# Kernel optimization log

Hardware: AMD Instinct MI355X
Metric: run time of the kernel (lower is better)

The kernel has to match this reference:

```python
import jax, jax.numpy as jnp
import numpy as np
import math

N = 20000      # nodes
E = 640000     # edges (avg degree 32)
G = 128        # g_dim (input features)
H1 = 128       # rgcn output dim
H2 = 128       # transformer output dim
R = 8          # num_relations


def setup_inputs() -> dict:
    key = jax.random.key(0)
    ks = jax.random.split(key, 12)
    x = jax.random.normal(ks[0], (N, G), dtype=jnp.float32)
    edge_index = jax.random.randint(ks[1], (2, E), 0, N)
    edge_type = jax.random.randint(ks[2], (E,), 0, R)
    s_in = 1.0 / math.sqrt(G)
    s_h1 = 1.0 / math.sqrt(H1)
    return {
        'x': x,
        'edge_index': edge_index,
        'edge_type': edge_type,
        # RGCNConv params (per-relation weights + root weight + bias)
        'rgcn_weight': jax.random.normal(ks[3], (R, G, H1), dtype=jnp.float32) * s_in,
        'rgcn_root': jax.random.normal(ks[4], (G, H1), dtype=jnp.float32) * s_in,
        'rgcn_bias': jnp.zeros((H1,), dtype=jnp.float32),
        # TransformerConv params (heads=1): query/key/value + skip linear
        'Wq': jax.random.normal(ks[5], (H1, H2), dtype=jnp.float32) * s_h1,
        'bq': jnp.zeros((H2,), dtype=jnp.float32),
        'Wk': jax.random.normal(ks[6], (H1, H2), dtype=jnp.float32) * s_h1,
        'bk': jnp.zeros((H2,), dtype=jnp.float32),
        'Wv': jax.random.normal(ks[7], (H1, H2), dtype=jnp.float32) * s_h1,
        'bv': jnp.zeros((H2,), dtype=jnp.float32),
        'Ws': jax.random.normal(ks[8], (H1, H2), dtype=jnp.float32) * s_h1,
        'bs': jnp.zeros((H2,), dtype=jnp.float32),
    }


def reference(x, edge_index, edge_type, rgcn_weight, rgcn_root, rgcn_bias,
              Wq, bq, Wk, bk, Wv, bv, Ws, bs):
    n = x.shape[0]
    src, dst = edge_index[0], edge_index[1]

    # ---- RGCNConv (aggr='mean' per relation, root weight + bias) ----
    # transform nodes by every relation, then gather per-edge message
    xr = jnp.einsum('ni,rio->nro', x, rgcn_weight)          # [N, R, H1]
    msg = xr[src, edge_type]                                # [E, H1]
    # per (dst, relation) edge counts for mean aggregation
    cnt = jnp.zeros((n, rgcn_weight.shape[0]), x.dtype).at[dst, edge_type].add(1.0)
    denom = jnp.maximum(cnt[dst, edge_type], 1.0)[:, None]  # [E, 1]
    agg = jnp.zeros((n, rgcn_weight.shape[2]), x.dtype).at[dst].add(msg / denom)
    h = agg + x @ rgcn_root + rgcn_bias
    h = jax.nn.relu(h)

    # ---- TransformerConv (heads=1, concat, root_weight=True) ----
    d = Wq.shape[1]
    q = h @ Wq + bq                                          # [N, H2]
    k = h @ Wk + bk
    v = h @ Wv + bv
    score = jnp.sum(q[dst] * k[src], axis=-1) / math.sqrt(d) # [E]
    # softmax over incoming edges of each destination node
    smax = jax.ops.segment_max(score, dst, num_segments=n)   # [N]
    e = jnp.exp(score - smax[dst])                           # [E]
    den = jax.ops.segment_sum(e, dst, num_segments=n)        # [N]
    alpha = e / jnp.maximum(den[dst], 1e-16)                 # [E]
    out = jax.ops.segment_sum(alpha[:, None] * v[src], dst, num_segments=n)
    out = out + h @ Ws + bs                                  # skip connection
    return jax.nn.relu(out)
```

## Files before the change

### kernel.cpp

```cpp
#include <hip/hip_runtime.h>

typedef unsigned short u16;
typedef unsigned int u32;
typedef __attribute__((ext_vector_type(8))) short short8;
typedef __attribute__((ext_vector_type(4))) float f32x4;

#define NN 20000
#define EE 640000
#define SCAN_BLOCKS 80

__device__ inline u16 f2bf(float f) {
    u32 x = __float_as_uint(f);
    return (u16)((x + 0x7FFFu + ((x >> 16) & 1u)) >> 16);
}
__device__ inline float lo16(u32 w) { return __uint_as_float(w << 16); }
__device__ inline float hi16(u32 w) { return __uint_as_float(w & 0xFFFF0000u); }
__device__ inline u32 packbf(float a, float b) { return ((u32)f2bf(b) << 16) | (u32)f2bf(a); }

#define CT_N (EE / 8)
#define CX_N (NN * 32)
#define WP_N (128 * 1152 + 4 * 128 * 128 + 512)
__global__ __launch_bounds__(256) void prep_count(const int* __restrict__ ei,
                                                  const int* __restrict__ et,
                                                  int* __restrict__ cnt, int* __restrict__ rank,
                                                  const float* __restrict__ x,
                                                  const float* rw, const float* root,
                                                  const float* Wq, const float* Wk,
                                                  const float* Wv, const float* Ws,
                                                  const float* bq, const float* bk,
                                                  const float* bv, const float* bs,
                                                  u16* __restrict__ xb,
                                                  u16* wt1, u16* wt2, float* bcat) {
    int idx = blockIdx.x * 256 + threadIdx.x;
    if (idx < CT_N) {
#pragma unroll
        for (int j = 0; j < 8; j++) {
            int e = idx + j * CT_N;
            int dst = ei[EE + e];
            int r = et[e];
            rank[e] = atomicAdd(&cnt[dst * 8 + r], 1);
        }
        return;
    }
    idx -= CT_N;
    if (idx < CX_N) {
        float4 v = *(const float4*)(x + (size_t)idx * 4);
        uint2 o;
        o.x = packbf(v.x, v.y);
        o.y = packbf(v.z, v.w);
        *(uint2*)(xb + (size_t)idx * 4) = o;
        return;
    }
    idx -= CX_N;
    const int S1 = 128 * 1152, S2 = 4 * 128 * 128;
    if (idx < S1) {
        int o = idx / 1152, k = idx - o * 1152;
        float v = (k < 1024) ? rw[k * 128 + o] : root[(k - 1024) * 128 + o];
        wt1[idx] = f2bf(v);
    } else if (idx < S1 + S2) {
        int j = idx - S1;
        int y = j >> 14, rem = j & 16383, o = rem >> 7, i = rem & 127;
        const float* W = (y == 0) ? Wq : (y == 1) ? Wk : (y == 2) ? Wv : Ws;
        wt2[j] = f2bf(W[i * 128 + o]);
    } else if (idx < S1 + S2 + 512) {
        int j = idx - (S1 + S2);
        int y = j >> 7, c = j & 127;
        const float* b = (y == 0) ? bq : (y == 1) ? bk : (y == 2) ? bv : bs;
        bcat[j] = b[c];
    }
}

__global__ __launch_bounds__(256) void scan_phase1(const int* __restrict__ cnt,
                                                   int* __restrict__ deg_pref,
                                                   int* __restrict__ blk_sums) {
    __shared__ int lds[256];
    int t = threadIdx.x;
    int n = blockIdx.x * 256 + t;
    int d = 0;
    if (n < NN) {
        int4 c0 = *(const int4*)(cnt + n * 8);
        int4 c1 = *(const int4*)(cnt + n * 8 + 4);
        d = c0.x + c0.y + c0.z + c0.w + c1.x + c1.y + c1.z + c1.w;
    }
    lds[t] = d;
    __syncthreads();
    for (int o = 1; o < 256; o <<= 1) {
        int v = (t >= o) ? lds[t - o] : 0;
        __syncthreads();
        lds[t] += v;
        __syncthreads();
    }
    if (n < NN) deg_pref[n] = lds[t];
    if (t == 255) blk_sums[blockIdx.x] = lds[255];
}

__global__ __launch_bounds__(256) void scan_phase3(const int* __restrict__ cnt,
                                                   const int* __restrict__ deg_pref,
                                                   const int* __restrict__ blk_sums,
                                                   int* __restrict__ row_off,
                                                   int* __restrict__ srt) {
    __shared__ int bs_lds[128];
    int t = threadIdx.x;
    if (t < 128) {
        int v = (t < SCAN_BLOCKS) ? blk_sums[t] : 0;
        bs_lds[t] = v;
    }
    __syncthreads();
    if (t < 128) {
        for (int o = 1; o < 128; o <<= 1) {
            int a = (t >= o) ? bs_lds[t - o] : 0;
            __syncthreads();
            bs_lds[t] += a;
            __syncthreads();
        }
    } else {
        for (int o = 1; o < 128; o <<= 1) {
            __syncthreads();
            __syncthreads();
        }
    }
    int blk_excl = (blockIdx.x > 0) ? bs_lds[blockIdx.x - 1] : 0;
    int n = blockIdx.x * 256 + t;
    if (n >= NN) return;
    int4 c0 = *(const int4*)(cnt + n * 8);
    int4 c1 = *(const int4*)(cnt + n * 8 + 4);
    int deg = c0.x + c0.y + c0.z + c0.w + c1.x + c1.y + c1.z + c1.w;
    int start = blk_excl + deg_pref[n] - deg;
    row_off[n] = start;
    int sub = start;
    int o[8];
    o[0] = sub; sub += c0.x;
    o[1] = sub; sub += c0.y;
    o[2] = sub; sub += c0.z;
    o[3] = sub; sub += c0.w;
    o[4] = sub; sub += c1.x;
    o[5] = sub; sub += c1.y;
    o[6] = sub; sub += c1.z;
    o[7] = sub; sub += c1.w;
    *(int4*)(srt + n * 8) = make_int4(o[0], o[1], o[2], o[3]);
    *(int4*)(srt + n * 8 + 4) = make_int4(o[4], o[5], o[6], o[7]);
    if (n == NN - 1) row_off[NN] = sub;
}

__global__ void scatter_kernel(const int* __restrict__ ei, const int* __restrict__ et,
                               const int* __restrict__ srt, const int* __restrict__ rank,
                               int* __restrict__ es) {
    int base = blockIdx.x * 2048 + threadIdx.x;
#pragma unroll
    for (int j = 0; j < 8; j++) {
        int e = base + j * 256;
        if (e < EE) {
            int dst = ei[EE + e];
            int src = ei[e];
            int r = et[e];
            es[srt[dst * 8 + r] + rank[e]] = src;
        }
    }
}

__global__ __launch_bounds__(256) void gemm_rgcn_fused(const u16* __restrict__ xb,
                                                       const int* __restrict__ srt,
                                                       const int* __restrict__ cnt,
                                                       const int* __restrict__ es,
                                                       const u16* __restrict__ Bt1,
                                                       const float* __restrict__ bias1,
                                                       const u16* __restrict__ Wt2,
                                                       const float* __restrict__ bcat,
                                                       u16* __restrict__ Cq, u16* __restrict__ Ckv,
                                                       u16* __restrict__ Cs) {
    __shared__ u16 As[2][16 * 136];
    int tid = threadIdx.x;
    int w = tid >> 6;
    int lane = tid & 63;
    int quad = lane >> 4;
    int ml = lane & 15;
    int nq = w;
    int block_m = blockIdx.x * 16;

    int node_l = tid >> 4;
    int th = tid & 15;
    int db = th * 8;
    int gnode = block_m + node_l;

    const u16* bp0 = Bt1 + (long)(nq * 32 + ml) * 1152 + quad * 8;

    f32x4 acc[2];
#pragma unroll
    for (int i = 0; i < 2; i++) acc[i] = (f32x4){0.f, 0.f, 0.f, 0.f};

#pragma unroll 1
    for (int slot = 0; slot < 9; slot++) {
        short8 bf[4][2];
#pragma unroll
        for (int ks = 0; ks < 4; ks++)
#pragma unroll
            for (int nt = 0; nt < 2; nt++)
                bf[ks][nt] = *(const short8*)(bp0 + (long)nt * 16 * 1152 + slot * 128 + ks * 32);

        u16* dst = &As[slot & 1][node_l * 136 + db];
        if (slot < 8) {
            int c = cnt[gnode * 8 + slot];
            int p0 = srt[gnode * 8 + slot];
            float a0 = 0.f, a1 = 0.f, a2 = 0.f, a3 = 0.f, a4 = 0.f, a5 = 0.f, a6 = 0.f, a7 = 0.f;
            int i = 0;
            for (; i + 2 <= c; i += 2) {
                int s0 = es[p0 + i], s1 = es[p0 + i + 1];
                uint4 wa = *(const uint4*)(xb + (long)s0 * 128 + db);
                uint4 wb = *(const uint4*)(xb + (long)s1 * 128 + db);
                a0 += lo16(wa.x) + lo16(wb.x);
                a1 += hi16(wa.x) + hi16(wb.x);
                a2 += lo16(wa.y) + lo16(wb.y);
                a3 += hi16(wa.y) + hi16(wb.y);
                a4 += lo16(wa.z) + lo16(wb.z);
                a5 += hi16(wa.z) + hi16(wb.z);
                a6 += lo16(wa.w) + lo16(wb.w);
                a7 += hi16(wa.w) + hi16(wb.w);
            }
            if (i < c) {
                int s0 = es[p0 + i];
                uint4 wa = *(const uint4*)(xb + (long)s0 * 128 + db);
                a0 += lo16(wa.x); a1 += hi16(wa.x); a2 += lo16(wa.y); a3 += hi16(wa.y);
                a4 += lo16(wa.z); a5 += hi16(wa.z); a6 += lo16(wa.w); a7 += hi16(wa.w);
            }
            float inv = 1.0f / (float)(c > 1 ? c : 1);
            uint4 o0 = make_uint4(packbf(a0 * inv, a1 * inv), packbf(a2 * inv, a3 * inv),
                                  packbf(a4 * inv, a5 * inv), packbf(a6 * inv, a7 * inv));
            *(uint4*)dst = o0;
        } else {
            short8 val = *(const short8*)(xb + (long)gnode * 128 + db);
            *(short8*)dst = val;
        }
        __syncthreads();
        const u16* ab = &As[slot & 1][0];
#pragma unroll
        for (int ks = 0; ks < 4; ks++) {
            short8 af = *(const short8*)(ab + ml * 136 + ks * 32 + quad * 8);
            acc[0] = __builtin_amdgcn_mfma_f32_16x16x32_bf16(af, bf[ks][0], acc[0], 0, 0, 0);
            acc[1] = __builtin_amdgcn_mfma_f32_16x16x32_bf16(af, bf[ks][1], acc[1], 0, 0, 0);
        }
    }
    __syncthreads();

#pragma unroll
    for (int nt = 0; nt < 2; nt++) {
        int col = nq * 32 + nt * 16 + ml;
        float bv = bias1[col];
#pragma unroll
        for (int i = 0; i < 4; i++) {
            int r = quad * 4 + i;
            As[0][r * 136 + col] = f2bf(fmaxf(acc[nt][i] + bv, 0.f));
        }
    }
    __syncthreads();

#pragma unroll 1
    for (int y = 0; y < 4; y++) {
        const u16* wp = Wt2 + (long)y * 16384 + (long)(nq * 32 + ml) * 128 + quad * 8;
        short8 bf2[4][2];
#pragma unroll
        for (int ks = 0; ks < 4; ks++)
#pragma unroll
            for (int nt = 0; nt < 2; nt++)
                bf2[ks][nt] = *(const short8*)(wp + (long)nt * 16 * 128 + ks * 32);
        f32x4 acc2[2];
#pragma unroll
        for (int i = 0; i < 2; i++) acc2[i] = (f32x4){0.f, 0.f, 0.f, 0.f};
#pragma unroll
        for (int ks = 0; ks < 4; ks++) {
            short8 af = *(const short8*)(&As[0][ml * 136 + ks * 32 + quad * 8]);
            acc2[0] = __builtin_amdgcn_mfma_f32_16x16x32_bf16(af, bf2[ks][0], acc2[0], 0, 0, 0);
            acc2[1] = __builtin_amdgcn_mfma_f32_16x16x32_bf16(af, bf2[ks][1], acc2[1], 0, 0, 0);
        }
        u16* C;
        int ldc;
        if (y == 0) { C = Cq; ldc = 128; }
        else if (y == 1) { C = Ckv; ldc = 256; }
        else if (y == 2) { C = Ckv + 128; ldc = 256; }
        else { C = Cs; ldc = 128; }
#pragma unroll
        for (int nt = 0; nt < 2; nt++) {
            int col = nq * 32 + nt * 16 + ml;
            float bv = bcat[y * 128 + col];
#pragma unroll
            for (int i = 0; i < 4; i++) {
                int gr = block_m + quad * 4 + i;
                C[(long)gr * ldc + col] = f2bf(acc2[nt][i] + bv);
            }
        }
    }
}

__global__ __launch_bounds__(128) void attn_kernel(const u16* __restrict__ q,
                                                   const u16* __restrict__ kv,
                                                   const u16* __restrict__ skip,
                                                   const int* __restrict__ row_off,
                                                   const int* __restrict__ es,
                                                   float* __restrict__ out) {
    int node = blockIdx.x * 8 + (threadIdx.x >> 4);
    int lane = threadIdx.x & 15;
    if (node >= NN) return;
    int p0 = row_off[node], p1 = row_off[node + 1];
    uint4 qw = *(const uint4*)(q + (long)node * 128 + lane * 8);
    float q0 = lo16(qw.x), q1 = hi16(qw.x), q2 = lo16(qw.y), q3 = hi16(qw.y);
    float q4 = lo16(qw.z), q5 = hi16(qw.z), q6 = lo16(qw.w), q7 = hi16(qw.w);
    const float SC = 0.08838834764831845f;
    float l = 0.f;
    float a0 = 0.f, a1 = 0.f, a2 = 0.f, a3 = 0.f, a4 = 0.f, a5 = 0.f, a6 = 0.f, a7 = 0.f;
    int p = p0;
    for (; p + 4 <= p1; p += 4) {
        const u16* b0 = kv + (long)es[p] * 256 + lane * 8;
        const u16* b1 = kv + (long)es[p + 1] * 256 + lane * 8;
        const u16* b2 = kv + (long)es[p + 2] * 256 + lane * 8;
        const u16* b3 = kv + (long)es[p + 3] * 256 + lane * 8;
        uint4 k0 = *(const uint4*)b0;
        uint4 k1 = *(const uint4*)b1;
        uint4 k2 = *(const uint4*)b2;
        uint4 k3 = *(const uint4*)b3;
        uint4 v0 = *(const uint4*)(b0 + 128);
        uint4 v1 = *(const uint4*)(b1 + 128);
        uint4 v2 = *(const uint4*)(b2 + 128);
        uint4 v3 = *(const uint4*)(b3 + 128);
        float t0 = q0 * lo16(k0.x) + q1 * hi16(k0.x) + q2 * lo16(k0.y) + q3 * hi16(k0.y) +
                   q4 * lo16(k0.z) + q5 * hi16(k0.z) + q6 * lo16(k0.w) + q7 * hi16(k0.w);
        float t1 = q0 * lo16(k1.x) + q1 * hi16(k1.x) + q2 * lo16(k1.y) + q3 * hi16(k1.y) +
                   q4 * lo16(k1.z) + q5 * hi16(k1.z) + q6 * lo16(k1.w) + q7 * hi16(k1.w);
        float t2 = q0 * lo16(k2.x) + q1 * hi16(k2.x) + q2 * lo16(k2.y) + q3 * hi16(k2.y) +
                   q4 * lo16(k2.z) + q5 * hi16(k2.z) + q6 * lo16(k2.w) + q7 * hi16(k2.w);
        float t3 = q0 * lo16(k3.x) + q1 * hi16(k3.x) + q2 * lo16(k3.y) + q3 * hi16(k3.y) +
                   q4 * lo16(k3.z) + q5 * hi16(k3.z) + q6 * lo16(k3.w) + q7 * hi16(k3.w);
#pragma unroll
        for (int off = 8; off >= 1; off >>= 1) {
            t0 += __shfl_xor(t0, off, 16);
            t1 += __shfl_xor(t1, off, 16);
            t2 += __shfl_xor(t2, off, 16);
            t3 += __shfl_xor(t3, off, 16);
        }
        float w0 = __expf(fminf(t0 * SC, 70.f));
        float w1 = __expf(fminf(t1 * SC, 70.f));
        float w2 = __expf(fminf(t2 * SC, 70.f));
        float w3 = __expf(fminf(t3 * SC, 70.f));
        l += (w0 + w1) + (w2 + w3);
        a0 += w0 * lo16(v0.x) + w1 * lo16(v1.x) + w2 * lo16(v2.x) + w3 * lo16(v3.x);
        a1 += w0 * hi16(v0.x) + w1 * hi16(v1.x) + w2 * hi16(v2.x) + w3 * hi16(v3.x);
        a2 += w0 * lo16(v0.y) + w1 * lo16(v1.y) + w2 * lo16(v2.y) + w3 * lo16(v3.y);
        a3 += w0 * hi16(v0.y) + w1 * hi16(v1.y) + w2 * hi16(v2.y) + w3 * hi16(v3.y);
        a4 += w0 * lo16(v0.z) + w1 * lo16(v1.z) + w2 * lo16(v2.z) + w3 * lo16(v3.z);
        a5 += w0 * hi16(v0.z) + w1 * hi16(v1.z) + w2 * hi16(v2.z) + w3 * hi16(v3.z);
        a6 += w0 * lo16(v0.w) + w1 * lo16(v1.w) + w2 * lo16(v2.w) + w3 * lo16(v3.w);
        a7 += w0 * hi16(v0.w) + w1 * hi16(v1.w) + w2 * hi16(v2.w) + w3 * hi16(v3.w);
    }
    for (; p < p1; p++) {
        const u16* b = kv + (long)es[p] * 256 + lane * 8;
        uint4 kw = *(const uint4*)b;
        uint4 vw = *(const uint4*)(b + 128);
        float t = q0 * lo16(kw.x) + q1 * hi16(kw.x) + q2 * lo16(kw.y) + q3 * hi16(kw.y) +
                  q4 * lo16(kw.z) + q5 * hi16(kw.z) + q6 * lo16(kw.w) + q7 * hi16(kw.w);
#pragma unroll
        for (int off = 8; off >= 1; off >>= 1) t += __shfl_xor(t, off, 16);
        float w = __expf(fminf(t * SC, 70.f));
        l += w;
        a0 += w * lo16(vw.x);
        a1 += w * hi16(vw.x);
        a2 += w * lo16(vw.y);
        a3 += w * hi16(vw.y);
        a4 += w * lo16(vw.z);
        a5 += w * hi16(vw.z);
        a6 += w * lo16(vw.w);
        a7 += w * hi16(vw.w);
    }
    float invl = (l > 0.f) ? 1.0f / l : 0.f;
    uint4 sw = *(const uint4*)(skip + (long)node * 128 + lane * 8);
    float4 oa, ob;
    oa.x = fmaxf(a0 * invl + lo16(sw.x), 0.f);
    oa.y = fmaxf(a1 * invl + hi16(sw.x), 0.f);
    oa.z = fmaxf(a2 * invl + lo16(sw.y), 0.f);
    oa.w = fmaxf(a3 * invl + hi16(sw.y), 0.f);
    ob.x = fmaxf(a4 * invl + lo16(sw.z), 0.f);
    ob.y = fmaxf(a5 * invl + hi16(sw.z), 0.f);
    ob.z = fmaxf(a6 * invl + lo16(sw.w), 0.f);
    ob.w = fmaxf(a7 * invl + hi16(sw.w), 0.f);
    *(float4*)(out + (long)node * 128 + lane * 8) = oa;
    *(float4*)(out + (long)node * 128 + lane * 8 + 4) = ob;
}

extern "C" void kernel_launch(void* const* d_in, const int* in_sizes, int n_in,
                              void* d_out, int out_size, void* d_ws, size_t ws_size,
                              hipStream_t stream) {
    const float* x = (const float*)d_in[0];
    const int* ei = (const int*)d_in[1];
    const int* et = (const int*)d_in[2];
    const float* rw = (const float*)d_in[3];
    const float* root = (const float*)d_in[4];
    const float* rbias = (const float*)d_in[5];
    const float* Wq = (const float*)d_in[6];
    const float* bq = (const float*)d_in[7];
    const float* Wk = (const float*)d_in[8];
    const float* bk = (const float*)d_in[9];
    const float* Wv = (const float*)d_in[10];
    const float* bv = (const float*)d_in[11];
    const float* Ws = (const float*)d_in[12];
    const float* bs = (const float*)d_in[13];

    char* ws = (char*)d_ws;
    size_t off = 0;
    auto alloc = [&](size_t b) {
        size_t o = off;
        off = (off + b + 255) & ~(size_t)255;
        return o;
    };
    u16* qv = (u16*)(ws + alloc((size_t)NN * 128 * 2));
    u16* kv = (u16*)(ws + alloc((size_t)NN * 256 * 2));
    u16* skip = (u16*)(ws + alloc((size_t)NN * 128 * 2));
    u16* xb = (u16*)(ws + alloc((size_t)NN * 128 * 2));
    u16* wt1 = (u16*)(ws + alloc((size_t)128 * 1152 * 2));
    u16* wt2 = (u16*)(ws + alloc((size_t)4 * 128 * 128 * 2));
    float* bcat = (float*)(ws + alloc((size_t)512 * 4));
    int* cnt = (int*)(ws + alloc((size_t)NN * 8 * 4));
    int* row_off = (int*)(ws + alloc((size_t)(NN + 1) * 4));
    int* srt = (int*)(ws + alloc((size_t)NN * 8 * 4));
    int* deg_pref = (int*)(ws + alloc((size_t)NN * 4));
    int* blk_sums = (int*)(ws + alloc((size_t)128 * 4));
    int* rank = (int*)(ws + alloc((size_t)EE * 4));
    int* es = (int*)(ws + alloc((size_t)EE * 4));
    (void)ws_size;
    (void)in_sizes;
    (void)n_in;
    (void)out_size;

    hipMemsetAsync(cnt, 0, (size_t)NN * 8 * 4, stream);

    prep_count<<<(CT_N + CX_N + WP_N + 255) / 256, 256, 0, stream>>>(
        ei, et, cnt, rank, x, rw, root, Wq, Wk, Wv, Ws, bq, bk, bv, bs,
        xb, wt1, wt2, bcat);

    scan_phase1<<<SCAN_BLOCKS, 256, 0, stream>>>(cnt, deg_pref, blk_sums);
    scan_phase3<<<SCAN_BLOCKS, 256, 0, stream>>>(cnt, deg_pref, blk_sums, row_off, srt);
    scatter_kernel<<<(EE + 2047) / 2048, 256, 0, stream>>>(ei, et, srt, rank, es);

    gemm_rgcn_fused<<<NN / 16, 256, 0, stream>>>(xb, srt, cnt, es, wt1, rbias, wt2, bcat,
                                                 qv, kv, skip);

    attn_kernel<<<(NN + 7) / 8, 128, 0, stream>>>(qv, kv, skip, row_off, es, (float*)d_out);
}
```

Measured before the change: 260.6 us.

## Gather all relation slots in parallel before MFMA loop with 512-thread blocks

Result: no change. 258.3 us (-0.9%).

```diff
diff --git a/kernel.cpp b/kernel.cpp
--- a/kernel.cpp
+++ b/kernel.cpp
@@ -158,7 +158,7 @@
     }
 }
 
-__global__ __launch_bounds__(256) void gemm_rgcn_fused(const u16* __restrict__ xb,
+__global__ __launch_bounds__(512) void gemm_rgcn_fused(const u16* __restrict__ xb,
                                                        const int* __restrict__ srt,
                                                        const int* __restrict__ cnt,
                                                        const int* __restrict__ es,
@@ -168,108 +168,132 @@
                                                        const float* __restrict__ bcat,
                                                        u16* __restrict__ Cq, u16* __restrict__ Ckv,
                                                        u16* __restrict__ Cs) {
-    __shared__ u16 As[2][16 * 136];
+    __shared__ u16 As[16 * 1224];
     int tid = threadIdx.x;
     int w = tid >> 6;
     int lane = tid & 63;
     int quad = lane >> 4;
     int ml = lane & 15;
-    int nq = w;
     int block_m = blockIdx.x * 16;
 
-    int node_l = tid >> 4;
-    int th = tid & 15;
-    int db = th * 8;
-    int gnode = block_m + node_l;
-
-    const u16* bp0 = Bt1 + (long)(nq * 32 + ml) * 1152 + quad * 8;
-
-    f32x4 acc[2];
-#pragma unroll
-    for (int i = 0; i < 2; i++) acc[i] = (f32x4){0.f, 0.f, 0.f, 0.f};
-
+    const u16* bp = Bt1 + (long)(w * 16 + ml) * 1152 + quad * 8;
+
+    short8 bf[4], bfn[4];
+#pragma unroll
+    for (int ks = 0; ks < 4; ks++) bf[ks] = *(const short8*)(bp + ks * 32);
+
+    {
+        int pair = tid >> 2;
+        int sub = tid & 3;
+        int node_l = pair >> 3;
+        int slot = pair & 7;
+        int gnode = block_m + node_l;
+        int c = cnt[gnode * 8 + slot];
+        int p0 = srt[gnode * 8 + slot];
+        float a[32];
+#pragma unroll
+        for (int j = 0; j < 32; j++) a[j] = 0.f;
+        const u16* xs = xb + sub * 32;
+        int i = 0;
+        for (; i + 2 <= c; i += 2) {
+            const u16* r0 = xs + (long)es[p0 + i] * 128;
+            const u16* r1 = xs + (long)es[p0 + i + 1] * 128;
+            uint4 wa[4], wb[4];
+#pragma unroll
+            for (int k = 0; k < 4; k++) wa[k] = *(const uint4*)(r0 + k * 8);
+#pragma unroll
+            for (int k = 0; k < 4; k++) wb[k] = *(const uint4*)(r1 + k * 8);
+#pragma unroll
+            for (int k = 0; k < 4; k++) {
+                a[k * 8 + 0] += lo16(wa[k].x) + lo16(wb[k].x);
+                a[k * 8 + 1] += hi16(wa[k].x) + hi16(wb[k].x);
+                a[k * 8 + 2] += lo16(wa[k].y) + lo16(wb[k].y);
+                a[k * 8 + 3] += hi16(wa[k].y) + hi16(wb[k].y);
+                a[k * 8 + 4] += lo16(wa[k].z) + lo16(wb[k].z);
+                a[k * 8 + 5] += hi16(wa[k].z) + hi16(wb[k].z);
+                a[k * 8 + 6] += lo16(wa[k].w) + lo16(wb[k].w);
+                a[k * 8 + 7] += hi16(wa[k].w) + hi16(wb[k].w);
+            }
+        }
+        if (i < c) {
+            const u16* r0 = xs + (long)es[p0 + i] * 128;
+#pragma unroll
+            for (int k = 0; k < 4; k++) {
+                uint4 wa = *(const uint4*)(r0 + k * 8);
+                a[k * 8 + 0] += lo16(wa.x);
+                a[k * 8 + 1] += hi16(wa.x);
+                a[k * 8 + 2] += lo16(wa.y);
+                a[k * 8 + 3] += hi16(wa.y);
+                a[k * 8 + 4] += lo16(wa.z);
+                a[k * 8 + 5] += hi16(wa.z);
+                a[k * 8 + 6] += lo16(wa.w);
+                a[k * 8 + 7] += hi16(wa.w);
+            }
+        }
+        float inv = 1.0f / (float)(c > 1 ? c : 1);
+        u16* dst = As + node_l * 1224 + slot * 136 + sub * 32;
+#pragma unroll
+        for (int k = 0; k < 4; k++) {
+            uint4 o = make_uint4(packbf(a[k * 8 + 0] * inv, a[k * 8 + 1] * inv),
+                                 packbf(a[k * 8 + 2] * inv, a[k * 8 + 3] * inv),
+                                 packbf(a[k * 8 + 4] * inv, a[k * 8 + 5] * inv),
+                                 packbf(a[k * 8 + 6] * inv, a[k * 8 + 7] * inv));
+            *(uint4*)(dst + k * 8) = o;
+        }
+    }
+    if (tid < 256) {
+        int r = tid >> 4;
+        int cb = (tid & 15) * 8;
+        short8 val = *(const short8*)(xb + (long)(block_m + r) * 128 + cb);
+        *(short8*)(As + r * 1224 + 8 * 136 + cb) = val;
+    }
+    __syncthreads();
+
+    f32x4 acc = (f32x4){0.f, 0.f, 0.f, 0.f};
 #pragma unroll 1
     for (int slot = 0; slot < 9; slot++) {
-        short8 bf[4][2];
-#pragma unroll
-        for (int ks = 0; ks < 4; ks++)
-#pragma unroll
-            for (int nt = 0; nt < 2; nt++)
-                bf[ks][nt] = *(const short8*)(bp0 + (long)nt * 16 * 1152 + slot * 128 + ks * 32);
-
-        u16* dst = &As[slot & 1][node_l * 136 + db];
         if (slot < 8) {
-            int c = cnt[gnode * 8 + slot];
-            int p0 = srt[gnode * 8 + slot];
-            float a0 = 0.f, a1 = 0.f, a2 = 0.f, a3 = 0.f, a4 = 0.f, a5 = 0.f, a6 = 0.f, a7 = 0.f;
-            int i = 0;
-            for (; i + 2 <= c; i += 2) {
-                int s0 = es[p0 + i], s1 = es[p0 + i + 1];
-                uint4 wa = *(const uint4*)(xb + (long)s0 * 128 + db);
-                uint4 wb = *(const uint4*)(xb + (long)s1 * 128 + db);
-                a0 += lo16(wa.x) + lo16(wb.x);
-                a1 += hi16(wa.x) + hi16(wb.x);
-                a2 += lo16(wa.y) + lo16(wb.y);
-                a3 += hi16(wa.y) + hi16(wb.y);
-                a4 += lo16(wa.z) + lo16(wb.z);
-                a5 += hi16(wa.z) + hi16(wb.z);
-                a6 += lo16(wa.w) + lo16(wb.w);
-                a7 += hi16(wa.w) + hi16(wb.w);
-            }
-            if (i < c) {
-                int s0 = es[p0 + i];
-                uint4 wa = *(const uint4*)(xb + (long)s0 * 128 + db);
-                a0 += lo16(wa.x); a1 += hi16(wa.x); a2 += lo16(wa.y); a3 += hi16(wa.y);
-                a4 += lo16(wa.z); a5 += hi16(wa.z); a6 += lo16(wa.w); a7 += hi16(wa.w);
-            }
-            float inv = 1.0f / (float)(c > 1 ? c : 1);
-            uint4 o0 = make_uint4(packbf(a0 * inv, a1 * inv), packbf(a2 * inv, a3 * inv),
-                                  packbf(a4 * inv, a5 * inv), packbf(a6 * inv, a7 * inv));
-            *(uint4*)dst = o0;
-        } else {
-            short8 val = *(const short8*)(xb + (long)gnode * 128 + db);
-            *(short8*)dst = val;
-        }
-        __syncthreads();
-        const u16* ab = &As[slot & 1][0];
+#pragma unroll
+            for (int ks = 0; ks < 4; ks++)
+                bfn[ks] = *(const short8*)(bp + (slot + 1) * 128 + ks * 32);
+        }
 #pragma unroll
         for (int ks = 0; ks < 4; ks++) {
-            short8 af = *(const short8*)(ab + ml * 136 + ks * 32 + quad * 8);
-            acc[0] = __builtin_amdgcn_mfma_f32_16x16x32_bf16(af, bf[ks][0], acc[0], 0, 0, 0);
-            acc[1] = __builtin_amdgcn_mfma_f32_16x16x32_bf16(af, bf[ks][1], acc[1], 0, 0, 0);
-        }
-    }
+            short8 af = *(const short8*)(As + ml * 1224 + slot * 136 + ks * 32 + quad * 8);
+            acc = __builtin_amdgcn_mfma_f32_16x16x32_bf16(af, bf[ks], acc, 0, 0, 0);
+        }
+#pragma unroll
+        for (int ks = 0; ks < 4; ks++) bf[ks] = bfn[ks];
+    }
+
+    const u16* wp = Wt2 + (long)(w * 16 + ml) * 128 + quad * 8;
+#pragma unroll
+    for (int ks = 0; ks < 4; ks++) bfn[ks] = *(const short8*)(wp + ks * 32);
+
     __syncthreads();
-
-#pragma unroll
-    for (int nt = 0; nt < 2; nt++) {
-        int col = nq * 32 + nt * 16 + ml;
+    {
+        int col = w * 16 + ml;
         float bv = bias1[col];
 #pragma unroll
-        for (int i = 0; i < 4; i++) {
-            int r = quad * 4 + i;
-            As[0][r * 136 + col] = f2bf(fmaxf(acc[nt][i] + bv, 0.f));
-        }
+        for (int i = 0; i < 4; i++)
+            As[(quad * 4 + i) * 1224 + col] = f2bf(fmaxf(acc[i] + bv, 0.f));
     }
     __syncthreads();
 
 #pragma unroll 1
     for (int y = 0; y < 4; y++) {
-        const u16* wp = Wt2 + (long)y * 16384 + (long)(nq * 32 + ml) * 128 + quad * 8;
-        short8 bf2[4][2];
-#pragma unroll
-        for (int ks = 0; ks < 4; ks++)
-#pragma unroll
-            for (int nt = 0; nt < 2; nt++)
-                bf2[ks][nt] = *(const short8*)(wp + (long)nt * 16 * 128 + ks * 32);
-        f32x4 acc2[2];
-#pragma unroll
-        for (int i = 0; i < 2; i++) acc2[i] = (f32x4){0.f, 0.f, 0.f, 0.f};
+#pragma unroll
+        for (int ks = 0; ks < 4; ks++) bf[ks] = bfn[ks];
+        if (y < 3) {
+#pragma unroll
+            for (int ks = 0; ks < 4; ks++)
+                bfn[ks] = *(const short8*)(wp + (long)(y + 1) * 16384 + ks * 32);
+        }
+        f32x4 acc2 = (f32x4){0.f, 0.f, 0.f, 0.f};
 #pragma unroll
         for (int ks = 0; ks < 4; ks++) {
-            short8 af = *(const short8*)(&As[0][ml * 136 + ks * 32 + quad * 8]);
-            acc2[0] = __builtin_amdgcn_mfma_f32_16x16x32_bf16(af, bf2[ks][0], acc2[0], 0, 0, 0);
-            acc2[1] = __builtin_amdgcn_mfma_f32_16x16x32_bf16(af, bf2[ks][1], acc2[1], 0, 0, 0);
+            short8 af = *(const short8*)(As + ml * 1224 + ks * 32 + quad * 8);
+            acc2 = __builtin_amdgcn_mfma_f32_16x16x32_bf16(af, bf[ks], acc2, 0, 0, 0);
         }
         u16* C;
         int ldc;
@@ -277,15 +301,12 @@
         else if (y == 1) { C = Ckv; ldc = 256; }
         else if (y == 2) { C = Ckv + 128; ldc = 256; }
         else { C = Cs; ldc = 128; }
-#pragma unroll
-        for (int nt = 0; nt < 2; nt++) {
-            int col = nq * 32 + nt * 16 + ml;
-            float bv = bcat[y * 128 + col];
-#pragma unroll
-            for (int i = 0; i < 4; i++) {
-                int gr = block_m + quad * 4 + i;
-                C[(long)gr * ldc + col] = f2bf(acc2[nt][i] + bv);
-            }
+        int col = w * 16 + ml;
+        float bv = bcat[y * 128 + col];
+#pragma unroll
+        for (int i = 0; i < 4; i++) {
+            int gr = block_m + quad * 4 + i;
+            C[(long)gr * ldc + col] = f2bf(acc2[i] + bv);
         }
     }
 }
@@ -437,7 +458,7 @@
     scan_phase3<<<SCAN_BLOCKS, 256, 0, stream>>>(cnt, deg_pref, blk_sums, row_off, srt);
     scatter_kernel<<<(EE + 2047) / 2048, 256, 0, stream>>>(ei, et, srt, rank, es);
 
-    gemm_rgcn_fused<<<NN / 16, 256, 0, stream>>>(xb, srt, cnt, es, wt1, rbias, wt2, bcat,
+    gemm_rgcn_fused<<<NN / 16, 512, 0, stream>>>(xb, srt, cnt, es, wt1, rbias, wt2, bcat,
                                                  qv, kv, skip);
 
     attn_kernel<<<(NN + 7) / 8, 128, 0, stream>>>(qv, kv, skip, row_off, es, (float*)d_out);
```
